# Kernel tuning notes

Measured on AMD Instinct MI355X. Metric: run time of the kernel, lower is better.

Reference implementation:

```python
import jax, jax.numpy as jnp
import numpy as np

N_PATHS = 8
T2_EFF = 0.5 * 100.0 + 0.5 * (100 // 50)  # p_dimer*T2_dimer + p_trimer*T2_trimer = 51.0
J_FREQ = 20.0


def setup_inputs() -> dict:
    key = jax.random.key(0)
    ks = jax.random.split(key, 5)
    B, D, H, P = 2048, 1024, 1024, N_PATHS
    return {
        "x": jax.random.normal(ks[0], (B, D), dtype=jnp.float32),
        "W_input": jax.random.normal(ks[1], (D, H), dtype=jnp.float32) * 0.1,
        "W_paths": jax.random.normal(ks[2], (P, H, H), dtype=jnp.float32) * 0.1,
        "J_coupling": jax.random.normal(ks[3], (P, P), dtype=jnp.float32) * 0.01,
        "coherent_state": jax.random.normal(ks[4], (B, P, H), dtype=jnp.float32),
        "t": jnp.ones((1,), dtype=jnp.float32),  # time_since_formation buffer
    }


def reference(x, W_input, W_paths, J_coupling, coherent_state, t):
    # base activation: [B, H]
    base = x @ W_input
    # all per-path matmuls batched into one einsum: [B, P, H]
    path_act = jnp.einsum("bh,phk->bpk", base, W_paths)
    # coherence decay gate (scalar, broadcasts)
    alpha = jnp.clip(jnp.exp(-t[0] / T2_EFF), 0.0, 1.0)
    superposition = alpha * coherent_state + (1.0 - alpha) * path_act
    # interference matrix from symmetrized J-coupling
    J_sym = 0.5 * (J_coupling + J_coupling.T)
    phase = 2.0 * jnp.pi * J_FREQ * t[0] / 1000.0
    interference = jax.nn.softmax(jnp.cos(phase * J_sym), axis=1)  # [P, P]
    # double-loop mixing == small matmul over path dim
    interfered = jnp.einsum("ij,bjh->bih", interference, superposition) / N_PATHS
    interfered = interfered * alpha  # coherence_factor == alpha
    # no measurement (default path): mean over paths
    return jnp.mean(interfered, axis=1)  # [B, H]
```

## Files before the change

### kernel.cpp

```cpp
#include <hip/hip_runtime.h>
#include <cstdint>


typedef __attribute__((ext_vector_type(8))) __bf16 bf16x8;
typedef __attribute__((ext_vector_type(4))) float f32x4;

__device__ __forceinline__ unsigned short f32_to_bf16_rne(float f) {
  unsigned int u = __float_as_uint(f);
  u += 0x7fffu + ((u >> 16) & 1u);
  return (unsigned short)(u >> 16);
}

__device__ __forceinline__ void load16_lds(const void* g, void* l) {
  __builtin_amdgcn_global_load_lds(
      (const __attribute__((address_space(1))) void*)g,
      (__attribute__((address_space(3))) void*)(unsigned int)(unsigned long long)l,
      16, 0, 0);
}

__global__ void k_scalars(const float* __restrict__ J, const float* __restrict__ t,
                          float* __restrict__ s) {
  const int lane = threadIdx.x;
  float tv = t[0];
  float alpha = expf(-tv / 51.0f);
  alpha = fminf(fmaxf(alpha, 0.0f), 1.0f);
  float phase = 2.0f * 3.14159265358979323846f * 20.0f * tv / 1000.0f;
  int i = lane >> 3, j = lane & 7;
  float jsym = 0.5f * (J[i * 8 + j] + J[j * 8 + i]);
  float e = expf(cosf(phase * jsym));
  float rs = e;
  rs += __shfl_xor(rs, 1);
  rs += __shfl_xor(rs, 2);
  rs += __shfl_xor(rs, 4);
  float p = e / rs;
  float cs = p;
  cs += __shfl_xor(cs, 8);
  cs += __shfl_xor(cs, 16);
  cs += __shfl_xor(cs, 32);
  float w = alpha * (1.0f / 64.0f) * cs;
  if (lane < 8) {
    s[lane] = w * (1.0f - alpha);
    s[8 + lane] = w * alpha;
  }
}

__global__ void k_convert(const float* __restrict__ x, const float* __restrict__ win,
                          unsigned short* __restrict__ xb, unsigned short* __restrict__ winb) {
  int idx = blockIdx.x * 256 + threadIdx.x;
  const float4* src;
  unsigned short* dst;
  int off;
  if (idx < 524288) { src = (const float4*)x;   dst = xb;   off = idx; }
  else              { src = (const float4*)win; dst = winb; off = idx - 524288; }
  float4 v = src[off];
  ushort4 o;
  o.x = f32_to_bf16_rne(v.x);
  o.y = f32_to_bf16_rne(v.y);
  o.z = f32_to_bf16_rne(v.z);
  o.w = f32_to_bf16_rne(v.w);
  ((ushort4*)dst)[off] = o;
}

__global__ void k_wefft(const float* __restrict__ Wp, const float* __restrict__ s,
                        unsigned short* __restrict__ wefft) {
  __shared__ float lt[32][33];
  const int tx = threadIdx.x;
  const int ty = threadIdx.y;
  const int k0 = blockIdx.x * 32;
  const int h0 = blockIdx.y * 32;
  float wj[8];
#pragma unroll
  for (int j = 0; j < 8; j++) wj[j] = s[j];
  float acc[4] = {0.f, 0.f, 0.f, 0.f};
#pragma unroll
  for (int j = 0; j < 8; j++) {
    const float* base = Wp + (size_t)j * 1024 * 1024;
#pragma unroll
    for (int r = 0; r < 4; r++) {
      int h1 = h0 + ty + 8 * r;
      acc[r] += wj[j] * base[(size_t)h1 * 1024 + k0 + tx];
    }
  }
#pragma unroll
  for (int r = 0; r < 4; r++) lt[ty + 8 * r][tx] = acc[r];
  __syncthreads();
#pragma unroll
  for (int r = 0; r < 4; r++) {
    float v = lt[tx][ty + 8 * r];
    wefft[(size_t)(k0 + ty + 8 * r) * 1024 + h0 + tx] = f32_to_bf16_rne(v);
  }
}

template <int MAIN>
__global__ __launch_bounds__(256) void k_gemm64(
    const unsigned short* __restrict__ A,
    const unsigned short* __restrict__ B,
    int K,
    float* __restrict__ outf,
    unsigned short* __restrict__ outb,
    const float* __restrict__ coh,
    const float* __restrict__ s) {
  __shared__ alignas(16) unsigned short As[64 * 32];
  __shared__ alignas(16) unsigned short Bs[64 * 32];
  const int m0 = blockIdx.x * 64;
  const int n0 = blockIdx.y * 64;
  const int tid = threadIdx.x;
  const int wave = tid >> 6;
  const int lane = tid & 63;
  const int quad = lane >> 4;
  const int t16 = lane & 15;

  const int srow = lane >> 2;
  const int sgrp = (lane & 3) ^ (srow & 3);
  const unsigned short* gA = A + (size_t)(m0 + wave * 16 + srow) * K + sgrp * 8;
  const unsigned short* gB = B + (size_t)(n0 + wave * 16 + srow) * K + sgrp * 8;
  unsigned short* lA = As + wave * 512 + lane * 8;
  unsigned short* lB = Bs + wave * 512 + lane * 8;

  const int wm = (wave >> 1) * 32;
  const int wn = (wave & 1) * 32;
  const int ar0 = wm + t16, ar1 = wm + 16 + t16;
  const int br0 = wn + t16, br1 = wn + 16 + t16;
  const unsigned short* pa0 = As + ar0 * 32 + ((quad ^ (ar0 & 3)) * 8);
  const unsigned short* pa1 = As + ar1 * 32 + ((quad ^ (ar1 & 3)) * 8);
  const unsigned short* pb0 = Bs + br0 * 32 + ((quad ^ (br0 & 3)) * 8);
  const unsigned short* pb1 = Bs + br1 * 32 + ((quad ^ (br1 & 3)) * 8);

  f32x4 acc00 = {0.f, 0.f, 0.f, 0.f}, acc01 = acc00, acc10 = acc00, acc11 = acc00;

  for (int kt = 0; kt < K; kt += 32) {
    __syncthreads();
    load16_lds(gA + kt, lA);
    load16_lds(gB + kt, lB);
    __syncthreads();
    bf16x8 a0 = *(const bf16x8*)pa0;
    bf16x8 a1 = *(const bf16x8*)pa1;
    bf16x8 b0 = *(const bf16x8*)pb0;
    bf16x8 b1 = *(const bf16x8*)pb1;
    acc00 = __builtin_amdgcn_mfma_f32_16x16x32_bf16(a0, b0, acc00, 0, 0, 0);
    acc01 = __builtin_amdgcn_mfma_f32_16x16x32_bf16(a0, b1, acc01, 0, 0, 0);
    acc10 = __builtin_amdgcn_mfma_f32_16x16x32_bf16(a1, b0, acc10, 0, 0, 0);
    acc11 = __builtin_amdgcn_mfma_f32_16x16x32_bf16(a1, b1, acc11, 0, 0, 0);
  }

  f32x4 accv[2][2] = {{acc00, acc01}, {acc10, acc11}};
  if constexpr (MAIN != 0) {
    float wA[8];
#pragma unroll
    for (int p = 0; p < 8; p++) wA[p] = s[8 + p];
#pragma unroll
    for (int i = 0; i < 2; i++) {
#pragma unroll
      for (int r = 0; r < 4; r++) {
        int m = m0 + wm + i * 16 + quad * 4 + r;
        const float* cb = coh + (size_t)m * 8192;
#pragma unroll
        for (int j = 0; j < 2; j++) {
          int n = n0 + wn + j * 16 + t16;
          float c = 0.f;
#pragma unroll
          for (int p = 0; p < 8; p++) c += wA[p] * cb[p * 1024 + n];
          outf[(size_t)m * 1024 + n] = accv[i][j][r] + c;
        }
      }
    }
  } else {
#pragma unroll
    for (int i = 0; i < 2; i++) {
#pragma unroll
      for (int r = 0; r < 4; r++) {
        int m = m0 + wm + i * 16 + quad * 4 + r;
#pragma unroll
        for (int j = 0; j < 2; j++) {
          int n = n0 + wn + j * 16 + t16;
          outb[(size_t)m * 1024 + n] = f32_to_bf16_rne(accv[i][j][r]);
        }
      }
    }
  }
}

extern "C" void kernel_launch(void* const* d_in, const int* in_sizes, int n_in,
                              void* d_out, int out_size, void* d_ws, size_t ws_size,
                              hipStream_t stream) {
  const float* x   = (const float*)d_in[0];
  const float* win = (const float*)d_in[1];
  const float* wp  = (const float*)d_in[2];
  const float* J   = (const float*)d_in[3];
  const float* coh = (const float*)d_in[4];
  const float* t   = (const float*)d_in[5];
  float* out = (float*)d_out;

  char* ws = (char*)d_ws;
  float* s              = (float*)ws;
  unsigned short* xb    = (unsigned short*)(ws + 64);
  unsigned short* winb  = (unsigned short*)(ws + 64 + 4u * 1024 * 1024);
  unsigned short* wefft = (unsigned short*)(ws + 64 + 6u * 1024 * 1024);
  unsigned short* wct   = (unsigned short*)(ws + 64 + 8u * 1024 * 1024);

  k_scalars<<<1, 64, 0, stream>>>(J, t, s);
  k_convert<<<3072, 256, 0, stream>>>(x, win, xb, winb);
  k_wefft<<<dim3(32, 32), dim3(32, 8), 0, stream>>>(wp, s, wefft);
  k_gemm64<0><<<dim3(16, 16), 256, 0, stream>>>(wefft, winb, 1024, nullptr, wct,
                                                nullptr, s);
  k_gemm64<1><<<dim3(32, 16), 256, 0, stream>>>(xb, wct, 1024, out, nullptr,
                                                coh, s);
}
```

Measured before the change: 182.5 us.

## Fuse prep kernels, enlarge GEMM tiles, overlap coherent-state reads with MFMA loop

Merges the scalar, convert and weight-fold kernels into one prep launch, with each block recomputing the scalars locally so no separate scalar kernel or global scalar buffer is needed. The GEMM now uses BK=64 and the main GEMM uses 128-row tiles. Coherent-state loads are spread across the K loop into register accumulators and staged through LDS for the epilogue. This cuts launch count and per-iteration barriers and hides the coherent-state bandwidth behind compute, at the cost of more registers and LDS per block and only 256 blocks for the main GEMM.

```diff
diff --git a/kernel.cpp b/kernel.cpp
--- a/kernel.cpp
+++ b/kernel.cpp
@@ -18,12 +18,12 @@
       16, 0, 0);
 }
 
-__global__ void k_scalars(const float* __restrict__ J, const float* __restrict__ t,
-                          float* __restrict__ s) {
-  const int lane = threadIdx.x;
+__device__ __forceinline__ void compute_scalars_wave(
+    const float* __restrict__ J, const float* __restrict__ t,
+    float* out_lo, float* out_hi) {
+  const int lane = threadIdx.x & 63;
   float tv = t[0];
-  float alpha = expf(-tv / 51.0f);
-  alpha = fminf(fmaxf(alpha, 0.0f), 1.0f);
+  float alpha = fminf(fmaxf(expf(-tv / 51.0f), 0.0f), 1.0f);
   float phase = 2.0f * 3.14159265358979323846f * 20.0f * tv / 1000.0f;
   int i = lane >> 3, j = lane & 7;
   float jsym = 0.5f * (J[i * 8 + j] + J[j * 8 + i]);
@@ -39,141 +39,199 @@
   cs += __shfl_xor(cs, 32);
   float w = alpha * (1.0f / 64.0f) * cs;
   if (lane < 8) {
-    s[lane] = w * (1.0f - alpha);
-    s[8 + lane] = w * alpha;
-  }
-}
-
-__global__ void k_convert(const float* __restrict__ x, const float* __restrict__ win,
-                          unsigned short* __restrict__ xb, unsigned short* __restrict__ winb) {
-  int idx = blockIdx.x * 256 + threadIdx.x;
-  const float4* src;
-  unsigned short* dst;
-  int off;
-  if (idx < 524288) { src = (const float4*)x;   dst = xb;   off = idx; }
-  else              { src = (const float4*)win; dst = winb; off = idx - 524288; }
-  float4 v = src[off];
-  ushort4 o;
-  o.x = f32_to_bf16_rne(v.x);
-  o.y = f32_to_bf16_rne(v.y);
-  o.z = f32_to_bf16_rne(v.z);
-  o.w = f32_to_bf16_rne(v.w);
-  ((ushort4*)dst)[off] = o;
-}
-
-__global__ void k_wefft(const float* __restrict__ Wp, const float* __restrict__ s,
-                        unsigned short* __restrict__ wefft) {
+    if (out_lo) out_lo[lane] = w * (1.0f - alpha);
+    if (out_hi) out_hi[lane] = w * alpha;
+  }
+}
+
+__global__ __launch_bounds__(256) void k_prep(
+    const float* __restrict__ x, const float* __restrict__ win,
+    const float* __restrict__ wp, const float* __restrict__ J,
+    const float* __restrict__ t, unsigned short* __restrict__ xb,
+    unsigned short* __restrict__ winb, unsigned short* __restrict__ wefft) {
+  __shared__ float sw[8];
   __shared__ float lt[32][33];
-  const int tx = threadIdx.x;
-  const int ty = threadIdx.y;
-  const int k0 = blockIdx.x * 32;
-  const int h0 = blockIdx.y * 32;
-  float wj[8];
-#pragma unroll
-  for (int j = 0; j < 8; j++) wj[j] = s[j];
-  float acc[4] = {0.f, 0.f, 0.f, 0.f};
-#pragma unroll
-  for (int j = 0; j < 8; j++) {
-    const float* base = Wp + (size_t)j * 1024 * 1024;
-#pragma unroll
-    for (int r = 0; r < 4; r++) {
-      int h1 = h0 + ty + 8 * r;
-      acc[r] += wj[j] * base[(size_t)h1 * 1024 + k0 + tx];
-    }
-  }
-#pragma unroll
-  for (int r = 0; r < 4; r++) lt[ty + 8 * r][tx] = acc[r];
-  __syncthreads();
-#pragma unroll
-  for (int r = 0; r < 4; r++) {
-    float v = lt[tx][ty + 8 * r];
-    wefft[(size_t)(k0 + ty + 8 * r) * 1024 + h0 + tx] = f32_to_bf16_rne(v);
-  }
-}
-
-template <int MAIN>
-__global__ __launch_bounds__(256) void k_gemm64(
-    const unsigned short* __restrict__ A,
-    const unsigned short* __restrict__ B,
-    int K,
-    float* __restrict__ outf,
-    unsigned short* __restrict__ outb,
-    const float* __restrict__ coh,
-    const float* __restrict__ s) {
-  __shared__ alignas(16) unsigned short As[64 * 32];
-  __shared__ alignas(16) unsigned short Bs[64 * 32];
-  const int m0 = blockIdx.x * 64;
-  const int n0 = blockIdx.y * 64;
+  const int blk = blockIdx.x;
+  const int tid = threadIdx.x;
+  if (blk < 3072) {
+    int idx = blk * 256 + tid;
+    const float4* src;
+    unsigned short* dst;
+    int off;
+    if (idx < 524288) { src = (const float4*)x;   dst = xb;   off = idx; }
+    else              { src = (const float4*)win; dst = winb; off = idx - 524288; }
+    float4 v = src[off];
+    ushort4 o;
+    o.x = f32_to_bf16_rne(v.x);
+    o.y = f32_to_bf16_rne(v.y);
+    o.z = f32_to_bf16_rne(v.z);
+    o.w = f32_to_bf16_rne(v.w);
+    ((ushort4*)dst)[off] = o;
+  } else {
+    if (tid < 64) compute_scalars_wave(J, t, sw, nullptr);
+    __syncthreads();
+    const int q = blk - 3072;
+    const int tx = tid & 31, ty = tid >> 5;
+    const int k0 = (q & 31) * 32, h0 = (q >> 5) * 32;
+    float acc[4] = {0.f, 0.f, 0.f, 0.f};
+#pragma unroll
+    for (int j = 0; j < 8; j++) {
+      const float* base = wp + (size_t)j * 1024 * 1024;
+      float wj = sw[j];
+#pragma unroll
+      for (int r = 0; r < 4; r++)
+        acc[r] += wj * base[(size_t)(h0 + ty + 8 * r) * 1024 + k0 + tx];
+    }
+#pragma unroll
+    for (int r = 0; r < 4; r++) lt[ty + 8 * r][tx] = acc[r];
+    __syncthreads();
+#pragma unroll
+    for (int r = 0; r < 4; r++)
+      wefft[(size_t)(k0 + ty + 8 * r) * 1024 + h0 + tx] =
+          f32_to_bf16_rne(lt[tx][ty + 8 * r]);
+  }
+}
+
+template <int BM, int MAIN>
+__global__ __launch_bounds__(256) void k_gemm(
+    const unsigned short* __restrict__ A, const unsigned short* __restrict__ B,
+    float* __restrict__ outf, unsigned short* __restrict__ outb,
+    const float* __restrict__ coh, const float* __restrict__ J,
+    const float* __restrict__ t) {
+  constexpr int K = 1024;
+  constexpr int BN = 64;
+  constexpr int BK = 64;
+  constexpr int FM = BM / 32;
+  constexpr int NA = BM / 32;
+  __shared__ alignas(16) unsigned short As[BM * BK];
+  __shared__ alignas(16) unsigned short Bs[BN * BK];
+  __shared__ float sm_s[8];
+  __shared__ float cohacc[MAIN ? BM * BN : 4];
+
+  const int m0 = blockIdx.x * BM;
+  const int n0 = blockIdx.y * BN;
   const int tid = threadIdx.x;
   const int wave = tid >> 6;
   const int lane = tid & 63;
   const int quad = lane >> 4;
   const int t16 = lane & 15;
 
-  const int srow = lane >> 2;
-  const int sgrp = (lane & 3) ^ (srow & 3);
-  const unsigned short* gA = A + (size_t)(m0 + wave * 16 + srow) * K + sgrp * 8;
-  const unsigned short* gB = B + (size_t)(n0 + wave * 16 + srow) * K + sgrp * 8;
-  unsigned short* lA = As + wave * 512 + lane * 8;
-  unsigned short* lB = Bs + wave * 512 + lane * 8;
-
-  const int wm = (wave >> 1) * 32;
+  float wA[8];
+  if constexpr (MAIN) {
+    if (tid < 64) compute_scalars_wave(J, t, nullptr, sm_s);
+    __syncthreads();
+#pragma unroll
+    for (int p = 0; p < 8; p++) wA[p] = sm_s[p];
+  }
+
+  const int srow = lane >> 3;
+  const int sgrp = lane & 7;
+  const unsigned short* gA[NA];
+  unsigned short* lA[NA];
+#pragma unroll
+  for (int c = 0; c < NA; c++) {
+    int r = (wave * NA + c) * 8 + srow;
+    int gcol = sgrp ^ (r & 7);
+    gA[c] = A + (size_t)(m0 + r) * K + gcol * 8;
+    lA[c] = As + (wave * NA + c) * 512 + lane * 8;
+  }
+  const unsigned short* gB[2];
+  unsigned short* lB[2];
+#pragma unroll
+  for (int c = 0; c < 2; c++) {
+    int r = (wave * 2 + c) * 8 + srow;
+    int gcol = sgrp ^ (r & 7);
+    gB[c] = B + (size_t)(n0 + r) * K + gcol * 8;
+    lB[c] = Bs + (wave * 2 + c) * 512 + lane * 8;
+  }
+
+  const int wm = (wave >> 1) * (BM / 2);
   const int wn = (wave & 1) * 32;
-  const int ar0 = wm + t16, ar1 = wm + 16 + t16;
-  const int br0 = wn + t16, br1 = wn + 16 + t16;
-  const unsigned short* pa0 = As + ar0 * 32 + ((quad ^ (ar0 & 3)) * 8);
-  const unsigned short* pa1 = As + ar1 * 32 + ((quad ^ (ar1 & 3)) * 8);
-  const unsigned short* pb0 = Bs + br0 * 32 + ((quad ^ (br0 & 3)) * 8);
-  const unsigned short* pb1 = Bs + br1 * 32 + ((quad ^ (br1 & 3)) * 8);
-
-  f32x4 acc00 = {0.f, 0.f, 0.f, 0.f}, acc01 = acc00, acc10 = acc00, acc11 = acc00;
-
-  for (int kt = 0; kt < K; kt += 32) {
-    __syncthreads();
-    load16_lds(gA + kt, lA);
-    load16_lds(gB + kt, lB);
-    __syncthreads();
-    bf16x8 a0 = *(const bf16x8*)pa0;
-    bf16x8 a1 = *(const bf16x8*)pa1;
-    bf16x8 b0 = *(const bf16x8*)pb0;
-    bf16x8 b1 = *(const bf16x8*)pb1;
-    acc00 = __builtin_amdgcn_mfma_f32_16x16x32_bf16(a0, b0, acc00, 0, 0, 0);
-    acc01 = __builtin_amdgcn_mfma_f32_16x16x32_bf16(a0, b1, acc01, 0, 0, 0);
-    acc10 = __builtin_amdgcn_mfma_f32_16x16x32_bf16(a1, b0, acc10, 0, 0, 0);
-    acc11 = __builtin_amdgcn_mfma_f32_16x16x32_bf16(a1, b1, acc11, 0, 0, 0);
-  }
-
-  f32x4 accv[2][2] = {{acc00, acc01}, {acc10, acc11}};
-  if constexpr (MAIN != 0) {
-    float wA[8];
-#pragma unroll
-    for (int p = 0; p < 8; p++) wA[p] = s[8 + p];
-#pragma unroll
-    for (int i = 0; i < 2; i++) {
-#pragma unroll
-      for (int r = 0; r < 4; r++) {
-        int m = m0 + wm + i * 16 + quad * 4 + r;
-        const float* cb = coh + (size_t)m * 8192;
-#pragma unroll
-        for (int j = 0; j < 2; j++) {
-          int n = n0 + wn + j * 16 + t16;
-          float c = 0.f;
-#pragma unroll
-          for (int p = 0; p < 8; p++) c += wA[p] * cb[p * 1024 + n];
-          outf[(size_t)m * 1024 + n] = accv[i][j][r] + c;
-        }
+  const unsigned short* pa[FM][2];
+  const unsigned short* pb[2][2];
+#pragma unroll
+  for (int mi = 0; mi < FM; mi++) {
+    int r = wm + mi * 16 + t16;
+#pragma unroll
+    for (int kk = 0; kk < 2; kk++)
+      pa[mi][kk] = As + r * BK + (((kk * 4 + quad) ^ (r & 7)) * 8);
+  }
+#pragma unroll
+  for (int ni = 0; ni < 2; ni++) {
+    int r = wn + ni * 16 + t16;
+#pragma unroll
+    for (int kk = 0; kk < 2; kk++)
+      pb[ni][kk] = Bs + r * BK + (((kk * 4 + quad) ^ (r & 7)) * 8);
+  }
+
+  f32x4 acc[FM][2];
+#pragma unroll
+  for (int mi = 0; mi < FM; mi++)
+#pragma unroll
+    for (int ni = 0; ni < 2; ni++) acc[mi][ni] = {0.f, 0.f, 0.f, 0.f};
+
+  f32x4 cacc[8];
+  const float* cbase = nullptr;
+  if constexpr (MAIN) {
+#pragma unroll
+    for (int s = 0; s < 8; s++) cacc[s] = {0.f, 0.f, 0.f, 0.f};
+    cbase = coh + (size_t)(m0 + (tid >> 4)) * 8192 + n0 + (tid & 15) * 4;
+  }
+
+  for (int it = 0; it < K / BK; it++) {
+    const int kt = it * BK;
+    __syncthreads();
+#pragma unroll
+    for (int c = 0; c < NA; c++) load16_lds(gA[c] + kt, lA[c]);
+#pragma unroll
+    for (int c = 0; c < 2; c++) load16_lds(gB[c] + kt, lB[c]);
+    if constexpr (MAIN) {
+      const int s = it >> 1, p0 = (it & 1) * 4;
+      const float* cp = cbase + (size_t)(s << 4) * 8192;
+#pragma unroll
+      for (int pp = 0; pp < 4; pp++) {
+        f32x4 v = *(const f32x4*)(cp + (p0 + pp) * 1024);
+        cacc[s] += wA[p0 + pp] * v;
       }
     }
-  } else {
-#pragma unroll
-    for (int i = 0; i < 2; i++) {
-#pragma unroll
-      for (int r = 0; r < 4; r++) {
-        int m = m0 + wm + i * 16 + quad * 4 + r;
-#pragma unroll
-        for (int j = 0; j < 2; j++) {
-          int n = n0 + wn + j * 16 + t16;
-          outb[(size_t)m * 1024 + n] = f32_to_bf16_rne(accv[i][j][r]);
+    __syncthreads();
+#pragma unroll
+    for (int kk = 0; kk < 2; kk++) {
+      bf16x8 a[FM], b[2];
+#pragma unroll
+      for (int mi = 0; mi < FM; mi++) a[mi] = *(const bf16x8*)pa[mi][kk];
+#pragma unroll
+      for (int ni = 0; ni < 2; ni++) b[ni] = *(const bf16x8*)pb[ni][kk];
+#pragma unroll
+      for (int mi = 0; mi < FM; mi++)
+#pragma unroll
+        for (int ni = 0; ni < 2; ni++)
+          acc[mi][ni] = __builtin_amdgcn_mfma_f32_16x16x32_bf16(
+              a[mi], b[ni], acc[mi][ni], 0, 0, 0);
+    }
+  }
+
+  if constexpr (MAIN) {
+    const int m_l = tid >> 4, nq = (tid & 15) * 4;
+#pragma unroll
+    for (int s = 0; s < 8; s++)
+      *(f32x4*)&cohacc[(m_l + (s << 4)) * BN + nq] = cacc[s];
+    __syncthreads();
+  }
+
+#pragma unroll
+  for (int mi = 0; mi < FM; mi++) {
+#pragma unroll
+    for (int r = 0; r < 4; r++) {
+      const int ml = wm + mi * 16 + quad * 4 + r;
+      const int m = m0 + ml;
+#pragma unroll
+      for (int ni = 0; ni < 2; ni++) {
+        const int nl = wn + ni * 16 + t16;
+        if constexpr (MAIN) {
+          outf[(size_t)m * 1024 + n0 + nl] = acc[mi][ni][r] + cohacc[ml * BN + nl];
+        } else {
+          outb[(size_t)m * 1024 + n0 + nl] = f32_to_bf16_rne(acc[mi][ni][r]);
         }
       }
     }
@@ -192,17 +250,14 @@
   float* out = (float*)d_out;
 
   char* ws = (char*)d_ws;
-  float* s              = (float*)ws;
-  unsigned short* xb    = (unsigned short*)(ws + 64);
-  unsigned short* winb  = (unsigned short*)(ws + 64 + 4u * 1024 * 1024);
-  unsigned short* wefft = (unsigned short*)(ws + 64 + 6u * 1024 * 1024);
-  unsigned short* wct   = (unsigned short*)(ws + 64 + 8u * 1024 * 1024);
-
-  k_scalars<<<1, 64, 0, stream>>>(J, t, s);
-  k_convert<<<3072, 256, 0, stream>>>(x, win, xb, winb);
-  k_wefft<<<dim3(32, 32), dim3(32, 8), 0, stream>>>(wp, s, wefft);
-  k_gemm64<0><<<dim3(16, 16), 256, 0, stream>>>(wefft, winb, 1024, nullptr, wct,
-                                                nullptr, s);
-  k_gemm64<1><<<dim3(32, 16), 256, 0, stream>>>(xb, wct, 1024, out, nullptr,
-                                                coh, s);
-}
+  unsigned short* xb    = (unsigned short*)ws;
+  unsigned short* winb  = (unsigned short*)(ws + 4u * 1024 * 1024);
+  unsigned short* wefft = (unsigned short*)(ws + 6u * 1024 * 1024);
+  unsigned short* wct   = (unsigned short*)(ws + 8u * 1024 * 1024);
+
+  k_prep<<<4096, 256, 0, stream>>>(x, win, wp, J, t, xb, winb, wefft);
+  k_gemm<64, 0><<<dim3(16, 16), 256, 0, stream>>>(wefft, winb, nullptr, wct,
+                                                  nullptr, nullptr, nullptr);
+  k_gemm<128, 1><<<dim3(16, 16), 256, 0, stream>>>(xb, wct, out, nullptr, coh,
+                                                   J, t);
+}
```

New measurement: 192.9 us. 5.7% more time.
